# Optimization experiments

Hardware: AMD Instinct MI355X
Metric: run time of the kernel (lower is better)

The kernel has to match this reference:

```python
import jax, jax.numpy as jnp
import numpy as np

A_PER_MOL = 32
N_MOL = 512
N_ATOMS = A_PER_MOL * N_MOL
F = 128
N_RBF = 20
L = 3
CUTOFF = 5.0
ACTION_SCALE = 1.0
ACTION_NORM_LIMIT = 1.0
EPS = 1e-8
MAX_Z = 100


def ssp(x):
    # shifted softplus used throughout schnetpack SchNet
    return jax.nn.softplus(x) - jnp.log(2.0)


def setup_inputs():
    key = jax.random.key(0)
    ks = jax.random.split(key, 12)
    positions = jax.random.normal(ks[0], (N_ATOMS, 3), jnp.float32) * 2.0
    Z = jax.random.randint(ks[1], (N_ATOMS,), 1, MAX_Z)
    # fully-connected intra-molecule neighbor lists (i != j)
    base = np.arange(A_PER_MOL)
    ii, jj = np.meshgrid(base, base, indexing='ij')
    m = ii != jj
    off = (np.arange(N_MOL) * A_PER_MOL)[:, None]
    idx_i = jnp.asarray((ii[m][None, :] + off).reshape(-1))
    idx_j = jnp.asarray((jj[m][None, :] + off).reshape(-1))
    mol_id = jnp.asarray(np.repeat(np.arange(N_MOL), A_PER_MOL))
    emb = jax.random.normal(ks[2], (MAX_Z, F)) * 0.1
    in2f_W = jax.random.normal(ks[3], (L, F, F)) * F ** -0.5
    filt_W1 = jax.random.normal(ks[4], (L, N_RBF, F)) * N_RBF ** -0.5
    filt_b1 = jnp.zeros((L, F))
    filt_W2 = jax.random.normal(ks[5], (L, F, F)) * F ** -0.5
    filt_b2 = jnp.zeros((L, F))
    f2out_W1 = jax.random.normal(ks[6], (L, F, F)) * F ** -0.5
    f2out_b1 = jnp.zeros((L, F))
    f2out_W2 = jax.random.normal(ks[7], (L, F, F)) * F ** -0.5
    f2out_b2 = jnp.zeros((L, F))
    aw_W1 = jax.random.normal(ks[8], (F, F // 2)) * F ** -0.5
    aw_b1 = jnp.zeros((F // 2,))
    aw_W2 = jax.random.normal(ks[9], (F // 2, 1)) * (F // 2) ** -0.5
    aw_b2 = jnp.zeros((1,))
    return dict(positions=positions, emb=emb, in2f_W=in2f_W, filt_W1=filt_W1,
                filt_b1=filt_b1, filt_W2=filt_W2, filt_b2=filt_b2,
                f2out_W1=f2out_W1, f2out_b1=f2out_b1, f2out_W2=f2out_W2,
                f2out_b2=f2out_b2, aw_W1=aw_W1, aw_b1=aw_b1, aw_W2=aw_W2,
                aw_b2=aw_b2, Z=Z, idx_i=idx_i, idx_j=idx_j, mol_id=mol_id)


def _energy(positions, emb, in2f_W, filt_W1, filt_b1, filt_W2, filt_b2,
            f2out_W1, f2out_b1, f2out_W2, f2out_b2, aw_W1, aw_b1, aw_W2,
            aw_b2, Z, idx_i, idx_j, mol_id):
    # PairwiseDistances
    rij = positions[idx_j] - positions[idx_i]                 # [E,3]
    d = jnp.sqrt(jnp.sum(rij * rij, axis=-1) + 1e-12)         # [E]
    # GaussianRBF(0..cutoff, n_rbf)
    offsets = jnp.linspace(0.0, CUTOFF, N_RBF)
    coeff = -0.5 / (offsets[1] - offsets[0]) ** 2
    rbf = jnp.exp(coeff * (d[:, None] - offsets) ** 2)        # [E,n_rbf]
    # CosineCutoff
    fcut = 0.5 * (jnp.cos(jnp.pi * d / CUTOFF) + 1.0) * (d < CUTOFF)
    x = emb[Z]                                                # [N,F]
    for l in range(L):  # SchNet interaction blocks
        h = x @ in2f_W[l]                                     # [N,F]
        Wf = ssp(rbf @ filt_W1[l] + filt_b1[l]) @ filt_W2[l] + filt_b2[l]
        msg = h[idx_j] * (Wf * fcut[:, None])                 # [E,F]
        agg = jax.ops.segment_sum(msg, idx_i, num_segments=N_ATOMS)
        x = x + (ssp(agg @ f2out_W1[l] + f2out_b1[l]) @ f2out_W2[l] + f2out_b2[l])
    # Atomwise energy head + per-molecule sum
    e_atom = (ssp(x @ aw_W1 + aw_b1) @ aw_W2 + aw_b2)[:, 0]   # [N]
    return jax.ops.segment_sum(e_atom, mol_id, num_segments=N_MOL)  # [M]


def reference(positions, emb, in2f_W, filt_W1, filt_b1, filt_W2, filt_b2,
              f2out_W1, f2out_b1, f2out_W2, f2out_b2, aw_W1, aw_b1, aw_W2,
              aw_b2, Z, idx_i, idx_j, mol_id):
    energy, vjp_fn = jax.vjp(
        lambda R: _energy(R, emb, in2f_W, filt_W1, filt_b1, filt_W2, filt_b2,
                          f2out_W1, f2out_b1, f2out_W2, f2out_b2, aw_W1,
                          aw_b1, aw_W2, aw_b2, Z, idx_i, idx_j, mol_id),
        positions)
    (gR,) = vjp_fn(jnp.ones_like(energy))
    action = (-gR) * ACTION_SCALE                             # anti_gradient (Forces module)
    # ragged per-molecule max-norm clip (segment version of the python loop)
    norms = jnp.sqrt(jnp.sum(action * action, axis=-1))       # [N]
    maxn = jax.ops.segment_max(norms, mol_id, num_segments=N_MOL)
    coef = jnp.minimum(ACTION_NORM_LIMIT / jnp.maximum(maxn, EPS), 1.0)
    action = action * coef[mol_id][:, None]
    return action, energy
```

## Files before the change

### kernel.cpp

```cpp
#include <hip/hip_runtime.h>
#include <cstddef>


#define FD     128
#define NRBF   20
#define CUTF   5.0f
#define PI_F   3.14159265358979f
#define PW     136
#define WLSZ   40960
#define W2LSZ  98304
#define APM    32

typedef unsigned short u16;
typedef unsigned int   u32;
typedef __attribute__((ext_vector_type(8))) short bf16x8;
typedef __attribute__((ext_vector_type(4))) float f32x4;

__device__ __forceinline__ float u16f(u16 x){ union{u32 i; float f;} v; v.i=((u32)x)<<16; return v.f; }
__device__ __forceinline__ u16 f16r(float f){ union{float f; u32 i;} v; v.f=f; u32 r=v.i+0x7fffu+((v.i>>16)&1u); return (u16)(r>>16); }
__device__ __forceinline__ float sspf(float x){
  return fmaxf(x,0.f) + __logf(1.f + __expf(-fabsf(x))) - 0.6931471805599453f;
}
__device__ __forceinline__ float sigf(float x){
  return __fdividef(1.f, 1.f + __expf(-x));
}
__device__ __forceinline__ float fcutf(float d){ return (d < CUTF) ? 0.5f*(__cosf(PI_F*d/CUTF)+1.f) : 0.f; }

__global__ __launch_bounds__(256) void k_zero(float* __restrict__ p, int n){
  int i = blockIdx.x*256 + threadIdx.x;
  if(i < n) p[i] = 0.f;
}

__global__ __launch_bounds__(256) void k_embed(const float* __restrict__ emb, const int* __restrict__ Z,
                                               float* __restrict__ X0, int n){
  int idx = blockIdx.x*256 + threadIdx.x;
  if(idx >= n) return;
  int a = idx >> 7, f = idx & 127;
  X0[idx] = emb[Z[a]*FD + f];
}

__global__ __launch_bounds__(256) void k_edge_geom(const float* __restrict__ pos,
    const int* __restrict__ Ii, const int* __restrict__ Ij,
    float* __restrict__ De, float* __restrict__ DBe, int E){
  int e = blockIdx.x*256 + threadIdx.x;
  if(e >= E) return;
  int i = Ii[e], j = Ij[e];
  float dx = pos[j*3+0]-pos[i*3+0];
  float dy = pos[j*3+1]-pos[i*3+1];
  float dz = pos[j*3+2]-pos[i*3+2];
  De[e] = sqrtf(dx*dx+dy*dy+dz*dz + 1e-12f);
  DBe[e] = 0.f;
}

__global__ __launch_bounds__(256) void k_prep(const float* __restrict__ fW1,
    const float* __restrict__ fW2, u16* __restrict__ WB){
  int idx = blockIdx.x*256 + threadIdx.x;
  if(idx >= 3*WLSZ) return;
  int l = idx / WLSZ, r = idx - l*WLSZ;
  const float* W1 = fW1 + l*2560;
  const float* W2 = fW2 + l*16384;
  u16* out = WB + l*WLSZ;
  if(r < 4096){
    int c = r >> 5, k = r & 31;
    out[r] = (k < NRBF) ? f16r(W1[k*128 + c]) : (u16)0;
  } else if(r < 8192){
    int rr = r - 4096;
    int k = rr >> 7, c = rr & 127;
    out[r] = (k < NRBF) ? f16r(W1[k*128 + c]) : (u16)0;
  } else if(r < 24576){
    out[r] = f16r(W2[r - 8192]);
  } else {
    int rr = r - 24576;
    int f = rr >> 7, c = rr & 127;
    out[r] = f16r(W2[c*128 + f]);
  }
}

__global__ __launch_bounds__(256) void k_prep2(const float* __restrict__ in2f,
    const float* __restrict__ oW1, const float* __restrict__ oW2,
    u16* __restrict__ WB2){
  int idx = blockIdx.x*256 + threadIdx.x;
  if(idx >= 3*W2LSZ) return;
  int l = idx / W2LSZ, r = idx - l*W2LSZ;
  int mat = r >> 14, q = r & 16383;
  int n = q >> 7, k = q & 127;
  const float* src = (mat < 2) ? (in2f + l*16384) : (mat < 4) ? (oW1 + l*16384) : (oW2 + l*16384);
  float v = (mat & 1) ? src[n*128 + k] : src[k*128 + n];
  WB2[idx] = f16r(v);
}

__global__ __launch_bounds__(256) void k_gemmb(const float* __restrict__ A,
    const u16* __restrict__ Bn, const float* __restrict__ bias,
    const float* __restrict__ res, const float* __restrict__ mul,
    float* __restrict__ out1, float* __restrict__ out2, int act, int Nr){
  __shared__ u16 sA[32*PW];
  const int tid = threadIdx.x;
  const int rb = blockIdx.x * 32;
  #pragma unroll
  for(int q=0;q<4;q++){
    int e = q*256 + tid;
    int r = e >> 5, c4 = (e & 31)*4;
    int rr = rb + r; if(rr >= Nr) rr = Nr-1;
    float4 v = *(const float4*)(A + (size_t)rr*FD + c4);
    sA[r*PW + c4+0] = f16r(v.x);
    sA[r*PW + c4+1] = f16r(v.y);
    sA[r*PW + c4+2] = f16r(v.z);
    sA[r*PW + c4+3] = f16r(v.w);
  }
  __syncthreads();
  const int w = tid >> 6, lane = tid & 63;
  const int quad = lane >> 4, l16 = lane & 15;
  f32x4 acc[2][2];
  #pragma unroll
  for(int mm=0;mm<2;mm++){ acc[mm][0]=(f32x4){0,0,0,0}; acc[mm][1]=(f32x4){0,0,0,0}; }
  #pragma unroll
  for(int ks=0;ks<4;ks++){
    bf16x8 va[2], vb[2];
    #pragma unroll
    for(int mm=0;mm<2;mm++)
      va[mm] = *(const bf16x8*)&sA[(mm*16+l16)*PW + ks*32 + quad*8];
    #pragma unroll
    for(int p=0;p<2;p++)
      vb[p] = *(const bf16x8*)(Bn + ((2*w+p)*16+l16)*128 + ks*32 + quad*8);
    #pragma unroll
    for(int mm=0;mm<2;mm++)
      #pragma unroll
      for(int p=0;p<2;p++)
        acc[mm][p] = __builtin_amdgcn_mfma_f32_16x16x32_bf16(va[mm], vb[p], acc[mm][p], 0,0,0);
  }
  #pragma unroll
  for(int mm=0;mm<2;mm++)
    #pragma unroll
    for(int p=0;p<2;p++){
      const int f = (2*w+p)*16 + l16;
      float bb = bias ? bias[f] : 0.f;
      #pragma unroll
      for(int r=0;r<4;r++){
        int row = rb + mm*16 + quad*4 + r;
        if(row >= Nr) continue;
        size_t o = (size_t)row*FD + f;
        float y = acc[mm][p][r] + bb;
        if(res) y += res[o];
        if(mul) y *= mul[o];
        if(act){ out1[o] = sspf(y); out2[o] = sigf(y); }
        else out1[o] = y;
      }
    }
}

__global__ __launch_bounds__(256) void k_edge_fwd8(
    const float* __restrict__ h,
    const float* __restrict__ De,
    const u16* __restrict__ W1t, const float* __restrict__ b1,
    const u16* __restrict__ W2t, const float* __restrict__ b2,
    float* __restrict__ agg, int EPM){
  __shared__ u16 srbfb[32*32];
  __shared__ u16 sP [32*PW];
  __shared__ u16 sWf[32*PW];
  __shared__ float sD[32];
  __shared__ float sRed[4*128];
  const int tid = threadIdx.x;
  const int nb = gridDim.x;
  const int P = ((nb & 7) == 0) ? ((blockIdx.x & 7)*(nb >> 3) + (blockIdx.x >> 3)) : blockIdx.x;
  const int m = P >> 5, a = P & 31;
  const int a0 = m*APM;
  const int eb = m*EPM + a*(APM-1);
  if(tid < 32) sD[tid] = (tid < APM-1) ? De[eb + tid] : (CUTF + 1.f);
  __syncthreads();
  const float step = CUTF/19.0f;
  const float coef = -0.5f/(step*step);
  {
    #pragma unroll
    for(int q=0;q<4;q++){
      int idx = q*256 + tid;
      int lt = idx >> 5, k = idx & 31;
      float x = sD[lt] - step*(float)k;
      srbfb[idx] = (k < NRBF) ? f16r(__expf(coef*x*x)) : (u16)0;
    }
  }
  __syncthreads();
  const int w = tid >> 6, lane = tid & 63;
  const int quad = lane >> 4, l16 = lane & 15;
  {
    f32x4 acc[2][2];
    #pragma unroll
    for(int mm=0;mm<2;mm++){ acc[mm][0]=(f32x4){0,0,0,0}; acc[mm][1]=(f32x4){0,0,0,0}; }
    bf16x8 va[2], vb[2];
    #pragma unroll
    for(int mm=0;mm<2;mm++)
      va[mm] = *(const bf16x8*)&srbfb[(mm*16+l16)*32 + quad*8];
    #pragma unroll
    for(int p=0;p<2;p++)
      vb[p] = *(const bf16x8*)(W1t + ((2*w+p)*16+l16)*32 + quad*8);
    #pragma unroll
    for(int mm=0;mm<2;mm++)
      #pragma unroll
      for(int p=0;p<2;p++)
        acc[mm][p] = __builtin_amdgcn_mfma_f32_16x16x32_bf16(va[mm], vb[p], acc[mm][p], 0,0,0);
    #pragma unroll
    for(int mm=0;mm<2;mm++)
      #pragma unroll
      for(int p=0;p<2;p++){
        const int c = (2*w+p)*16 + l16;
        float bb = b1[c];
        #pragma unroll
        for(int r=0;r<4;r++)
          sP[(mm*16+quad*4+r)*PW + c] = f16r(sspf(acc[mm][p][r] + bb));
      }
  }
  __syncthreads();
  {
    f32x4 acc[2][2];
    #pragma unroll
    for(int mm=0;mm<2;mm++){ acc[mm][0]=(f32x4){0,0,0,0}; acc[mm][1]=(f32x4){0,0,0,0}; }
    #pragma unroll
    for(int ks=0;ks<4;ks++){
      bf16x8 va[2], vb[2];
      #pragma unroll
      for(int mm=0;mm<2;mm++)
        va[mm] = *(const bf16x8*)&sP[(mm*16+l16)*PW + ks*32 + quad*8];
      #pragma unroll
      for(int p=0;p<2;p++)
        vb[p] = *(const bf16x8*)(W2t + ((2*w+p)*16+l16)*128 + ks*32 + quad*8);
      #pragma unroll
      for(int mm=0;mm<2;mm++)
        #pragma unroll
        for(int p=0;p<2;p++)
          acc[mm][p] = __builtin_amdgcn_mfma_f32_16x16x32_bf16(va[mm], vb[p], acc[mm][p], 0,0,0);
    }
    #pragma unroll
    for(int mm=0;mm<2;mm++)
      #pragma unroll
      for(int p=0;p<2;p++){
        const int f = (2*w+p)*16 + l16;
        float bb = b2[f];
        #pragma unroll
        for(int r=0;r<4;r++)
          sWf[(mm*16+quad*4+r)*PW + f] = f16r(acc[mm][p][r] + bb);
      }
  }
  __syncthreads();
  {
    float r0 = 0.f, r1 = 0.f;
    #pragma unroll
    for(int s=0;s<8;s++){
      int lt = w*8 + s;
      int j = (lt < APM-1) ? (lt + (lt >= a ? 1 : 0)) : 0;
      float fc = fcutf(sD[lt]);
      const float* hr = h + (size_t)(a0 + j)*FD;
      float w0 = u16f(sWf[lt*PW + lane]);
      float w1 = u16f(sWf[lt*PW + lane + 64]);
      r0 += hr[lane]      * w0 * fc;
      r1 += hr[lane + 64] * w1 * fc;
    }
    sRed[w*128 + lane]      = r0;
    sRed[w*128 + lane + 64] = r1;
  }
  __syncthreads();
  if(tid < 128){
    float v = sRed[tid] + sRed[128+tid] + sRed[256+tid] + sRed[384+tid];
    agg[(size_t)(a0+a)*FD + tid] = v;
  }
}

__global__ __launch_bounds__(256) void k_edge_bwd8(
    const float* __restrict__ h, const float* __restrict__ AB,
    const float* __restrict__ De,
    const u16* __restrict__ W1t, const float* __restrict__ b1,
    const u16* __restrict__ W1b, const u16* __restrict__ W2r,
    const u16* __restrict__ W2t, const float* __restrict__ b2,
    float* __restrict__ DBe, float* __restrict__ HB, int EPM){
  __shared__ u16 srbfb[32*32];
  __shared__ float srbf[32*NRBF];
  __shared__ u16 sP [32*PW];
  __shared__ u16 sWf[32*PW];
  __shared__ float sD[32];
  __shared__ float sRed[4*128];
  __shared__ float sdb[32*2];
  __shared__ float sfb[32];
  const int tid = threadIdx.x;
  const int nb = gridDim.x;
  const int P = ((nb & 7) == 0) ? ((blockIdx.x & 7)*(nb >> 3) + (blockIdx.x >> 3)) : blockIdx.x;
  const int m = P >> 5, a = P & 31;
  const int a0 = m*APM;
  const int eb = m*EPM + a*(APM-1);
  if(tid < 32) sD[tid] = (tid < APM-1) ? De[eb + tid] : (CUTF + 1.f);
  __syncthreads();
  const float step = CUTF/19.0f;
  const float coef = -0.5f/(step*step);
  {
    #pragma unroll
    for(int q=0;q<4;q++){
      int idx = q*256 + tid;
      int lt = idx >> 5, k = idx & 31;
      float x = sD[lt] - step*(float)k;
      if(k < NRBF){
        float v = __expf(coef*x*x);
        srbf[lt*NRBF + k] = v;
        srbfb[idx] = f16r(v);
      } else srbfb[idx] = (u16)0;
    }
  }
  __syncthreads();
  const int w = tid >> 6, lane = tid & 63;
  const int quad = lane >> 4, l16 = lane & 15;
  {
    f32x4 acc[2][2];
    #pragma unroll
    for(int mm=0;mm<2;mm++){ acc[mm][0]=(f32x4){0,0,0,0}; acc[mm][1]=(f32x4){0,0,0,0}; }
    bf16x8 va[2], vb[2];
    #pragma unroll
    for(int mm=0;mm<2;mm++)
      va[mm] = *(const bf16x8*)&srbfb[(mm*16+l16)*32 + quad*8];
    #pragma unroll
    for(int p=0;p<2;p++)
      vb[p] = *(const bf16x8*)(W1t + ((2*w+p)*16+l16)*32 + quad*8);
    #pragma unroll
    for(int mm=0;mm<2;mm++)
      #pragma unroll
      for(int p=0;p<2;p++)
        acc[mm][p] = __builtin_amdgcn_mfma_f32_16x16x32_bf16(va[mm], vb[p], acc[mm][p], 0,0,0);
    #pragma unroll
    for(int mm=0;mm<2;mm++)
      #pragma unroll
      for(int p=0;p<2;p++){
        const int c = (2*w+p)*16 + l16;
        float bb = b1[c];
        #pragma unroll
        for(int r=0;r<4;r++)
          sP[(mm*16+quad*4+r)*PW + c] = f16r(sspf(acc[mm][p][r] + bb));
      }
  }
  __syncthreads();
  {
    f32x4 acc[2][2];
    #pragma unroll
    for(int mm=0;mm<2;mm++){ acc[mm][0]=(f32x4){0,0,0,0}; acc[mm][1]=(f32x4){0,0,0,0}; }
    #pragma unroll
    for(int ks=0;ks<4;ks++){
      bf16x8 va[2], vb[2];
      #pragma unroll
      for(int mm=0;mm<2;mm++)
        va[mm] = *(const bf16x8*)&sP[(mm*16+l16)*PW + ks*32 + quad*8];
      #pragma unroll
      for(int p=0;p<2;p++)
        vb[p] = *(const bf16x8*)(W2t + ((2*w+p)*16+l16)*128 + ks*32 + quad*8);
      #pragma unroll
      for(int mm=0;mm<2;mm++)
        #pragma unroll
        for(int p=0;p<2;p++)
          acc[mm][p] = __builtin_amdgcn_mfma_f32_16x16x32_bf16(va[mm], vb[p], acc[mm][p], 0,0,0);
    }
    #pragma unroll
    for(int mm=0;mm<2;mm++)
      #pragma unroll
      for(int p=0;p<2;p++){
        const int f = (2*w+p)*16 + l16;
        float bb = b2[f];
        #pragma unroll
        for(int r=0;r<4;r++)
          sWf[(mm*16+quad*4+r)*PW + f] = f16r(acc[mm][p][r] + bb);
      }
  }
  __syncthreads();
  {
    float ab0 = AB[(size_t)(a0+a)*FD + lane];
    float ab1 = AB[(size_t)(a0+a)*FD + lane + 64];
    float r0 = 0.f, r1 = 0.f;
    float pfv[8];
    #pragma unroll
    for(int s=0;s<8;s++){
      int lt = w*8 + s;
      int j = (lt < APM-1) ? (lt + (lt >= a ? 1 : 0)) : 0;
      float fc = fcutf(sD[lt]);
      const float* hr  = h  + (size_t)(a0 + j)*FD;
      const float* abr = AB + (size_t)(a0 + j)*FD;
      float h0 = hr[lane], h1 = hr[lane + 64];
      float w0 = u16f(sWf[lt*PW + lane]);
      float w1 = u16f(sWf[lt*PW + lane + 64]);
      r0 += abr[lane]      * w0 * fc;
      r1 += abr[lane + 64] * w1 * fc;
      float g0 = ab0*h0, g1 = ab1*h1;
      sWf[lt*PW + lane]      = f16r(g0*fc);
      sWf[lt*PW + lane + 64] = f16r(g1*fc);
      pfv[s] = g0*w0 + g1*w1;
    }
    #pragma unroll
    for(int d2=1; d2<64; d2<<=1){
      #pragma unroll
      for(int s=0;s<8;s++) pfv[s] += __shfl_xor(pfv[s], d2);
    }
    if(lane == 0){
      #pragma unroll
      for(int s=0;s<8;s++) sfb[w*8 + s] = pfv[s];
    }
    sRed[w*128 + lane]      = r0;
    sRed[w*128 + lane + 64] = r1;
  }
  __syncthreads();
  if(tid < 128){
    float v = sRed[tid] + sRed[128+tid] + sRed[256+tid] + sRed[384+tid];
    HB[(size_t)(a0+a)*FD + tid] = v;
  }
  float tbv[2][2][4];
  {
    f32x4 acc[2][2];
    #pragma unroll
    for(int mm=0;mm<2;mm++){ acc[mm][0]=(f32x4){0,0,0,0}; acc[mm][1]=(f32x4){0,0,0,0}; }
    #pragma unroll
    for(int ks=0;ks<4;ks++){
      bf16x8 va[2], vb[2];
      #pragma unroll
      for(int mm=0;mm<2;mm++)
        va[mm] = *(const bf16x8*)&sWf[(mm*16+l16)*PW + ks*32 + quad*8];
      #pragma unroll
      for(int p=0;p<2;p++)
        vb[p] = *(const bf16x8*)(W2r + ((2*w+p)*16+l16)*128 + ks*32 + quad*8);
      #pragma unroll
      for(int mm=0;mm<2;mm++)
        #pragma unroll
        for(int p=0;p<2;p++)
          acc[mm][p] = __builtin_amdgcn_mfma_f32_16x16x32_bf16(va[mm], vb[p], acc[mm][p], 0,0,0);
    }
    #pragma unroll
    for(int mm=0;mm<2;mm++)
      #pragma unroll
      for(int p=0;p<2;p++){
        const int c = (2*w+p)*16 + l16;
        #pragma unroll
        for(int r=0;r<4;r++){
          float Pv = u16f(sP[(mm*16+quad*4+r)*PW + c]);
          float sig = 1.0f - 0.5f*__expf(-Pv);
          tbv[mm][p][r] = acc[mm][p][r] * sig;
        }
      }
  }
  __syncthreads();
  {
    #pragma unroll
    for(int mm=0;mm<2;mm++)
      #pragma unroll
      for(int p=0;p<2;p++){
        const int c = (2*w+p)*16 + l16;
        #pragma unroll
        for(int r=0;r<4;r++)
          sWf[(mm*16+quad*4+r)*PW + c] = f16r(tbv[mm][p][r]);
      }
  }
  __syncthreads();
  {
    const int m3 = w >> 1, p3 = w & 1;
    f32x4 acc = (f32x4){0,0,0,0};
    #pragma unroll
    for(int ks=0;ks<4;ks++){
      bf16x8 va = *(const bf16x8*)&sWf[(m3*16+l16)*PW + ks*32 + quad*8];
      bf16x8 vb = *(const bf16x8*)(W1b + (p3*16+l16)*128 + ks*32 + quad*8);
      acc = __builtin_amdgcn_mfma_f32_16x16x32_bf16(va, vb, acc, 0,0,0);
    }
    const int kr = p3*16 + l16;
    float s0[4];
    #pragma unroll
    for(int r=0;r<4;r++){
      int lt = m3*16 + quad*4 + r;
      float v = 0.f;
      if(kr < NRBF){
        float x = sD[lt] - step*(float)kr;
        v = acc[r] * srbf[lt*NRBF + kr] * (2.f*coef*x);
      }
      s0[r] = v;
    }
    #pragma unroll
    for(int d2=1; d2<16; d2<<=1){
      #pragma unroll
      for(int r=0;r<4;r++) s0[r] += __shfl_xor(s0[r], d2);
    }
    if(l16 == 0){
      #pragma unroll
      for(int r=0;r<4;r++) sdb[(m3*16+quad*4+r)*2 + p3] = s0[r];
    }
  }
  __syncthreads();
  if(tid < APM-1){
    const float d = sD[tid];
    float dfc = (d < CUTF) ? (-0.5f*(PI_F/CUTF)*__sinf(PI_F*d/CUTF)) : 0.f;
    DBe[eb + tid] += sdb[tid*2+0] + sdb[tid*2+1] + sfb[tid]*dfc;
  }
}

__global__ __launch_bounds__(256) void k_head(const float* __restrict__ X3,
    const float* __restrict__ aW1, const float* __restrict__ ab1,
    const float* __restrict__ aW2, const float* __restrict__ ab2,
    const int* __restrict__ mol, float* __restrict__ Emol, float* __restrict__ XB, int N){
  __shared__ float sx[64*129];
  __shared__ float sg[64*65];
  const int tid = threadIdx.x;
  const int base = blockIdx.x*64;
  for(int q=0;q<8;q++){
    int ee = q*256 + tid;
    int r = ee >> 5, c = (ee & 31)*4;
    int row = base + r; if(row >= N) row = N-1;
    float4 v = *(const float4*)(X3 + (size_t)row*FD + c);
    sx[r*129 + c+0] = v.x; sx[r*129 + c+1] = v.y;
    sx[r*129 + c+2] = v.z; sx[r*129 + c+3] = v.w;
  }
  __syncthreads();
  {
    const int a = tid >> 2, q = tid & 3;
    float u[16];
    #pragma unroll
    for(int cc=0;cc<16;cc++) u[cc] = ab1[q*16 + cc];
    for(int f=0; f<128; f++){
      float xv = sx[a*129 + f];
      const float4* wp = (const float4*)(aW1 + f*64 + q*16);
      float4 w0 = wp[0], w1 = wp[1], w2 = wp[2], w3 = wp[3];
      u[0]+=xv*w0.x; u[1]+=xv*w0.y; u[2]+=xv*w0.z; u[3]+=xv*w0.w;
      u[4]+=xv*w1.x; u[5]+=xv*w1.y; u[6]+=xv*w1.z; u[7]+=xv*w1.w;
      u[8]+=xv*w2.x; u[9]+=xv*w2.y; u[10]+=xv*w2.z; u[11]+=xv*w2.w;
      u[12]+=xv*w3.x; u[13]+=xv*w3.y; u[14]+=xv*w3.z; u[15]+=xv*w3.w;
    }
    float pe = 0.f;
    #pragma unroll
    for(int cc=0;cc<16;cc++){
      int c = q*16 + cc;
      pe += sspf(u[cc])*aW2[c];
      sg[a*65 + c] = sigf(u[cc])*aW2[c];
    }
    pe += __shfl_xor(pe, 1);
    pe += __shfl_xor(pe, 2);
    if(q == 0 && base + a < N) atomicAdd(&Emol[mol[base + a]], pe + ab2[0]);
  }
  __syncthreads();
  {
    const int f = tid & 127, g2 = tid >> 7;
    float acc[32];
    #pragma unroll
    for(int q=0;q<32;q++) acc[q]=0.f;
    for(int c=0;c<64;c++){
      float w = aW1[f*64 + c];
      #pragma unroll
      for(int q=0;q<32;q++) acc[q] += sg[(g2*32+q)*65 + c]*w;
    }
    #pragma unroll
    for(int q=0;q<32;q++){
      int row = base + g2*32 + q;
      if(row < N) XB[(size_t)row*FD + f] = acc[q];
    }
  }
}

__global__ __launch_bounds__(256) void k_grad(const float* __restrict__ pos,
    const int* __restrict__ Ii, const int* __restrict__ Ij,
    const float* __restrict__ De, const float* __restrict__ DBe,
    float* __restrict__ G, int E){
  int e = blockIdx.x*256 + threadIdx.x;
  if(e >= E) return;
  if(De[e] >= CUTF) return;
  float s = DBe[e] / De[e];
  int i = Ii[e], j = Ij[e];
  float dx = s*(pos[i*3+0]-pos[j*3+0]);
  float dy = s*(pos[i*3+1]-pos[j*3+1]);
  float dz = s*(pos[i*3+2]-pos[j*3+2]);
  atomicAdd(&G[i*3+0], dx); atomicAdd(&G[i*3+1], dy); atomicAdd(&G[i*3+2], dz);
  atomicAdd(&G[j*3+0], -dx); atomicAdd(&G[j*3+1], -dy); atomicAdd(&G[j*3+2], -dz);
}

__global__ __launch_bounds__(256) void k_norm(const float* __restrict__ G,
    const int* __restrict__ mol, u32* __restrict__ maxnU, int N){
  int n = blockIdx.x*256 + threadIdx.x;
  if(n >= N) return;
  float ax = G[n*3], ay = G[n*3+1], az = G[n*3+2];
  float nrm = sqrtf(ax*ax+ay*ay+az*az);
  atomicMax(&maxnU[mol[n]], __float_as_uint(nrm));
}

__global__ __launch_bounds__(256) void k_apply(const float* __restrict__ G,
    const int* __restrict__ mol, const u32* __restrict__ maxnU,
    float* __restrict__ outA, int N){
  int n = blockIdx.x*256 + threadIdx.x;
  if(n >= N) return;
  float mx = __uint_as_float(maxnU[mol[n]]);
  float coefc = fminf(1.0f/fmaxf(mx, 1e-8f), 1.0f);
  outA[n*3+0] = -G[n*3+0]*coefc;
  outA[n*3+1] = -G[n*3+1]*coefc;
  outA[n*3+2] = -G[n*3+2]*coefc;
}

extern "C" void kernel_launch(void* const* d_in, const int* in_sizes, int n_in,
                              void* d_out, int out_size, void* d_ws, size_t ws_size,
                              hipStream_t stream) {
  (void)n_in;
  const float* pos  = (const float*)d_in[0];
  const float* emb  = (const float*)d_in[1];
  const float* in2f = (const float*)d_in[2];
  const float* fW1  = (const float*)d_in[3];
  const float* fb1  = (const float*)d_in[4];
  const float* fW2  = (const float*)d_in[5];
  const float* fb2  = (const float*)d_in[6];
  const float* oW1  = (const float*)d_in[7];
  const float* ob1  = (const float*)d_in[8];
  const float* oW2  = (const float*)d_in[9];
  const float* ob2  = (const float*)d_in[10];
  const float* aW1  = (const float*)d_in[11];
  const float* ab1  = (const float*)d_in[12];
  const float* aW2  = (const float*)d_in[13];
  const float* ab2  = (const float*)d_in[14];
  const int*   Z    = (const int*)d_in[15];
  const int*   Ii   = (const int*)d_in[16];
  const int*   Ij   = (const int*)d_in[17];
  const int*   mol  = (const int*)d_in[18];
  const int N = in_sizes[15];
  const int E = in_sizes[16];
  const int M = out_size - N*3;
  const int EPM = E / M;
  const size_t NFE = (size_t)N*FD;
  float* outF = (float*)d_out;
  float* outE = outF + (size_t)N*3;
  float* ws = (float*)d_ws;
  if(ws_size < (11*NFE + 2*(size_t)E + 3*(WLSZ/2) + 3*(W2LSZ/2) + 64)*4) return;

  float* X0  = ws;
  float* SV0 = ws + 4*NFE;
  float* H   = ws + 7*NFE;
  float* AGG = ws + 8*NFE;
  float* XB  = ws + 9*NFE;
  float* HB  = ws + 10*NFE;
  float* De  = ws + 11*NFE;
  float* DBe = De + E;
  u16*   WB  = (u16*)(DBe + E);
  u16*   WB2 = WB + 3*WLSZ;
  float* G    = AGG;
  u32*  maxnU = (u32*)H;

  const int gN   = (int)((NFE + 255)/256);
  const int gE   = (E + 255)/256;
  const int gRow = (N + 31)/32;
  const int gHead= (N + 63)/64;

  k_embed<<<gN,256,0,stream>>>(emb, Z, X0, (int)NFE);
  k_edge_geom<<<gE,256,0,stream>>>(pos, Ii, Ij, De, DBe, E);
  k_prep<<<(3*WLSZ+255)/256,256,0,stream>>>(fW1, fW2, WB);
  k_prep2<<<(3*W2LSZ+255)/256,256,0,stream>>>(in2f, oW1, oW2, WB2);
  for(int l=0;l<3;l++){
    float* Xl  = X0 + (size_t)l*NFE;
    float* Xn  = X0 + (size_t)(l+1)*NFE;
    float* SVl = SV0 + (size_t)l*NFE;
    const u16* W1t = WB + l*WLSZ;
    const u16* W2t = W1t + 24576;
    const u16* d = WB2 + l*W2LSZ;
    const u16 *in2f_t = d, *oW1_t = d + 32768, *oW2_t = d + 65536;
    k_gemmb<<<gRow,256,0,stream>>>(Xl, in2f_t, nullptr, nullptr, nullptr, H, nullptr, 0, N);
    k_edge_fwd8<<<N,256,0,stream>>>(H, De, W1t, fb1 + l*128, W2t, fb2 + l*128, AGG, EPM);
    k_gemmb<<<gRow,256,0,stream>>>(AGG, oW1_t, ob1 + l*128, nullptr, nullptr, H, SVl, 1, N);
    k_gemmb<<<gRow,256,0,stream>>>(H, oW2_t, ob2 + l*128, Xl, nullptr, Xn, nullptr, 0, N);
  }
  k_zero<<<(M+255)/256,256,0,stream>>>(outE, M);
  k_head<<<gHead,256,0,stream>>>(X0 + 3*NFE, aW1, ab1, aW2, ab2, mol, outE, XB, N);
  for(int l=2;l>=0;l--){
    float* Xl  = X0 + (size_t)l*NFE;
    float* SVl = SV0 + (size_t)l*NFE;
    const u16* W1t = WB + l*WLSZ;
    const u16* W1b = W1t + 4096;
    const u16* W2r = W1t + 8192;
    const u16* W2t = W1t + 24576;
    const u16* d = WB2 + l*W2LSZ;
    const u16 *in2f_t = d, *in2f_d = d + 16384, *oW1_d = d + 49152, *oW2_d = d + 81920;
    k_gemmb<<<gRow,256,0,stream>>>(XB, oW2_d, nullptr, nullptr, SVl, AGG, nullptr, 0, N);
    k_gemmb<<<gRow,256,0,stream>>>(AGG, oW1_d, nullptr, nullptr, nullptr, AGG, nullptr, 0, N);
    k_gemmb<<<gRow,256,0,stream>>>(Xl, in2f_t, nullptr, nullptr, nullptr, H, nullptr, 0, N);
    k_edge_bwd8<<<N,256,0,stream>>>(H, AGG, De, W1t, fb1 + l*128, W1b, W2r, W2t, fb2 + l*128, DBe, HB, EPM);
    k_gemmb<<<gRow,256,0,stream>>>(HB, in2f_d, nullptr, XB, nullptr, XB, nullptr, 0, N);
  }
  k_zero<<<(N*3+255)/256,256,0,stream>>>(G, N*3);
  k_zero<<<(M+255)/256,256,0,stream>>>((float*)maxnU, M);
  k_grad<<<gE,256,0,stream>>>(pos, Ii, Ij, De, DBe, G, E);
  k_norm<<<(N+255)/256,256,0,stream>>>(G, mol, maxnU, N);
  k_apply<<<(N+255)/256,256,0,stream>>>(G, mol, maxnU, outF, N);
}
```

Baseline: 1.428 ms.

## Cache forward edge filter activations for reuse in backward edge kernel

The forward edge kernel now stores its per-edge pre-activation (sP) and filter (sWf) tiles in bf16 to a workspace buffer for each layer. A new backward kernel reloads these tiles instead of recomputing the RBF expansion and the two filter-network GEMMs. This trades recomputation for roughly 8 KB of extra global traffic per atom per layer and a large extra workspace allocation. The path is taken only when the workspace is big enough, and otherwise falls back to the old kernel.

```diff
diff --git a/kernel.cpp b/kernel.cpp
--- a/kernel.cpp
+++ b/kernel.cpp
@@ -153,7 +153,7 @@
     const float* __restrict__ De,
     const u16* __restrict__ W1t, const float* __restrict__ b1,
     const u16* __restrict__ W2t, const float* __restrict__ b2,
-    float* __restrict__ agg, int EPM){
+    float* __restrict__ agg, u16* __restrict__ PC, u16* __restrict__ WC, int EPM){
   __shared__ u16 srbfb[32*32];
   __shared__ u16 sP [32*PW];
   __shared__ u16 sWf[32*PW];
@@ -240,6 +240,17 @@
       }
   }
   __syncthreads();
+  if(WC){
+    u16* PCt = PC + (size_t)P*4096;
+    u16* WCt = WC + (size_t)P*4096;
+    #pragma unroll
+    for(int q=0;q<2;q++){
+      int idx = q*256 + tid;
+      int row = idx >> 4, c8 = (idx & 15)*8;
+      *(bf16x8*)(PCt + row*128 + c8) = *(const bf16x8*)&sP[row*PW + c8];
+      *(bf16x8*)(WCt + row*128 + c8) = *(const bf16x8*)&sWf[row*PW + c8];
+    }
+  }
   {
     float r0 = 0.f, r1 = 0.f;
     #pragma unroll
@@ -466,6 +477,166 @@
       if(kr < NRBF){
         float x = sD[lt] - step*(float)kr;
         v = acc[r] * srbf[lt*NRBF + kr] * (2.f*coef*x);
+      }
+      s0[r] = v;
+    }
+    #pragma unroll
+    for(int d2=1; d2<16; d2<<=1){
+      #pragma unroll
+      for(int r=0;r<4;r++) s0[r] += __shfl_xor(s0[r], d2);
+    }
+    if(l16 == 0){
+      #pragma unroll
+      for(int r=0;r<4;r++) sdb[(m3*16+quad*4+r)*2 + p3] = s0[r];
+    }
+  }
+  __syncthreads();
+  if(tid < APM-1){
+    const float d = sD[tid];
+    float dfc = (d < CUTF) ? (-0.5f*(PI_F/CUTF)*__sinf(PI_F*d/CUTF)) : 0.f;
+    DBe[eb + tid] += sdb[tid*2+0] + sdb[tid*2+1] + sfb[tid]*dfc;
+  }
+}
+
+__global__ __launch_bounds__(256) void k_edge_bwd9c(
+    const float* __restrict__ h, const float* __restrict__ AB,
+    const float* __restrict__ De,
+    const u16* __restrict__ PC, const u16* __restrict__ WC,
+    const u16* __restrict__ W1b, const u16* __restrict__ W2r,
+    float* __restrict__ DBe, float* __restrict__ HB, int EPM){
+  __shared__ u16 sP [32*PW];
+  __shared__ u16 sWf[32*PW];
+  __shared__ float sD[32];
+  __shared__ float sRed[4*128];
+  __shared__ float sdb[32*2];
+  __shared__ float sfb[32];
+  const int tid = threadIdx.x;
+  const int nb = gridDim.x;
+  const int P = ((nb & 7) == 0) ? ((blockIdx.x & 7)*(nb >> 3) + (blockIdx.x >> 3)) : blockIdx.x;
+  const int m = P >> 5, a = P & 31;
+  const int a0 = m*APM;
+  const int eb = m*EPM + a*(APM-1);
+  const u16* PCt = PC + (size_t)P*4096;
+  const u16* WCt = WC + (size_t)P*4096;
+  if(tid < 32) sD[tid] = (tid < APM-1) ? De[eb + tid] : (CUTF + 1.f);
+  {
+    #pragma unroll
+    for(int q=0;q<2;q++){
+      int idx = q*256 + tid;
+      int row = idx >> 4, c8 = (idx & 15)*8;
+      *(bf16x8*)&sP [row*PW + c8] = *(const bf16x8*)(PCt + row*128 + c8);
+      *(bf16x8*)&sWf[row*PW + c8] = *(const bf16x8*)(WCt + row*128 + c8);
+    }
+  }
+  __syncthreads();
+  const float step = CUTF/19.0f;
+  const float coef = -0.5f/(step*step);
+  const int w = tid >> 6, lane = tid & 63;
+  const int quad = lane >> 4, l16 = lane & 15;
+  {
+    float ab0 = AB[(size_t)(a0+a)*FD + lane];
+    float ab1 = AB[(size_t)(a0+a)*FD + lane + 64];
+    float r0 = 0.f, r1 = 0.f;
+    float pfv[8];
+    #pragma unroll
+    for(int s=0;s<8;s++){
+      int lt = w*8 + s;
+      int j = (lt < APM-1) ? (lt + (lt >= a ? 1 : 0)) : 0;
+      float fc = fcutf(sD[lt]);
+      const float* hr  = h  + (size_t)(a0 + j)*FD;
+      const float* abr = AB + (size_t)(a0 + j)*FD;
+      float h0 = hr[lane], h1 = hr[lane + 64];
+      float w0 = u16f(sWf[lt*PW + lane]);
+      float w1 = u16f(sWf[lt*PW + lane + 64]);
+      r0 += abr[lane]      * w0 * fc;
+      r1 += abr[lane + 64] * w1 * fc;
+      float g0 = ab0*h0, g1 = ab1*h1;
+      sWf[lt*PW + lane]      = f16r(g0*fc);
+      sWf[lt*PW + lane + 64] = f16r(g1*fc);
+      pfv[s] = g0*w0 + g1*w1;
+    }
+    #pragma unroll
+    for(int d2=1; d2<64; d2<<=1){
+      #pragma unroll
+      for(int s=0;s<8;s++) pfv[s] += __shfl_xor(pfv[s], d2);
+    }
+    if(lane == 0){
+      #pragma unroll
+      for(int s=0;s<8;s++) sfb[w*8 + s] = pfv[s];
+    }
+    sRed[w*128 + lane]      = r0;
+    sRed[w*128 + lane + 64] = r1;
+  }
+  __syncthreads();
+  if(tid < 128){
+    float v = sRed[tid] + sRed[128+tid] + sRed[256+tid] + sRed[384+tid];
+    HB[(size_t)(a0+a)*FD + tid] = v;
+  }
+  float tbv[2][2][4];
+  {
+    f32x4 acc[2][2];
+    #pragma unroll
+    for(int mm=0;mm<2;mm++){ acc[mm][0]=(f32x4){0,0,0,0}; acc[mm][1]=(f32x4){0,0,0,0}; }
+    #pragma unroll
+    for(int ks=0;ks<4;ks++){
+      bf16x8 va[2], vb[2];
+      #pragma unroll
+      for(int mm=0;mm<2;mm++)
+        va[mm] = *(const bf16x8*)&sWf[(mm*16+l16)*PW + ks*32 + quad*8];
+      #pragma unroll
+      for(int p=0;p<2;p++)
+        vb[p] = *(const bf16x8*)(W2r + ((2*w+p)*16+l16)*128 + ks*32 + quad*8);
+      #pragma unroll
+      for(int mm=0;mm<2;mm++)
+        #pragma unroll
+        for(int p=0;p<2;p++)
+          acc[mm][p] = __builtin_amdgcn_mfma_f32_16x16x32_bf16(va[mm], vb[p], acc[mm][p], 0,0,0);
+    }
+    #pragma unroll
+    for(int mm=0;mm<2;mm++)
+      #pragma unroll
+      for(int p=0;p<2;p++){
+        const int c = (2*w+p)*16 + l16;
+        #pragma unroll
+        for(int r=0;r<4;r++){
+          float Pv = u16f(sP[(mm*16+quad*4+r)*PW + c]);
+          float sig = 1.0f - 0.5f*__expf(-Pv);
+          tbv[mm][p][r] = acc[mm][p][r] * sig;
+        }
+      }
+  }
+  __syncthreads();
+  {
+    #pragma unroll
+    for(int mm=0;mm<2;mm++)
+      #pragma unroll
+      for(int p=0;p<2;p++){
+        const int c = (2*w+p)*16 + l16;
+        #pragma unroll
+        for(int r=0;r<4;r++)
+          sWf[(mm*16+quad*4+r)*PW + c] = f16r(tbv[mm][p][r]);
+      }
+  }
+  __syncthreads();
+  {
+    const int m3 = w >> 1, p3 = w & 1;
+    f32x4 acc = (f32x4){0,0,0,0};
+    #pragma unroll
+    for(int ks=0;ks<4;ks++){
+      bf16x8 va = *(const bf16x8*)&sWf[(m3*16+l16)*PW + ks*32 + quad*8];
+      bf16x8 vb = *(const bf16x8*)(W1b + (p3*16+l16)*128 + ks*32 + quad*8);
+      acc = __builtin_amdgcn_mfma_f32_16x16x32_bf16(va, vb, acc, 0,0,0);
+    }
+    const int kr = p3*16 + l16;
+    float s0[4];
+    #pragma unroll
+    for(int r=0;r<4;r++){
+      int lt = m3*16 + quad*4 + r;
+      float v = 0.f;
+      if(kr < NRBF){
+        float x = sD[lt] - step*(float)kr;
+        float rb = __expf(coef*x*x);
+        v = acc[r] * rb * (2.f*coef*x);
       }
       s0[r] = v;
     }
@@ -616,7 +787,10 @@
   float* outF = (float*)d_out;
   float* outE = outF + (size_t)N*3;
   float* ws = (float*)d_ws;
-  if(ws_size < (11*NFE + 2*(size_t)E + 3*(WLSZ/2) + 3*(W2LSZ/2) + 64)*4) return;
+  const size_t base_u32 = 11*NFE + 2*(size_t)E + 3*(WLSZ/2) + 3*(W2LSZ/2) + 64;
+  if(ws_size < base_u32*4) return;
+  const size_t CSZ = (size_t)N*4096;
+  const int fast = (ws_size >= (base_u32 + 3*CSZ + 16)*4);
 
   float* X0  = ws;
   float* SV0 = ws + 4*NFE;
@@ -628,6 +802,8 @@
   float* DBe = De + E;
   u16*   WB  = (u16*)(DBe + E);
   u16*   WB2 = WB + 3*WLSZ;
+  u16*   PC  = WB2 + 3*W2LSZ;
+  u16*   WC  = PC + 3*CSZ;
   float* G    = AGG;
   u32*  maxnU = (u32*)H;
 
@@ -648,8 +824,10 @@
     const u16* W2t = W1t + 24576;
     const u16* d = WB2 + l*W2LSZ;
     const u16 *in2f_t = d, *oW1_t = d + 32768, *oW2_t = d + 65536;
+    u16* PCl = fast ? (PC + l*CSZ) : (u16*)nullptr;
+    u16* WCl = fast ? (WC + l*CSZ) : (u16*)nullptr;
     k_gemmb<<<gRow,256,0,stream>>>(Xl, in2f_t, nullptr, nullptr, nullptr, H, nullptr, 0, N);
-    k_edge_fwd8<<<N,256,0,stream>>>(H, De, W1t, fb1 + l*128, W2t, fb2 + l*128, AGG, EPM);
+    k_edge_fwd8<<<N,256,0,stream>>>(H, De, W1t, fb1 + l*128, W2t, fb2 + l*128, AGG, PCl, WCl, EPM);
     k_gemmb<<<gRow,256,0,stream>>>(AGG, oW1_t, ob1 + l*128, nullptr, nullptr, H, SVl, 1, N);
     k_gemmb<<<gRow,256,0,stream>>>(H, oW2_t, ob2 + l*128, Xl, nullptr, Xn, nullptr, 0, N);
   }
@@ -667,7 +845,11 @@
     k_gemmb<<<gRow,256,0,stream>>>(XB, oW2_d, nullptr, nullptr, SVl, AGG, nullptr, 0, N);
     k_gemmb<<<gRow,256,0,stream>>>(AGG, oW1_d, nullptr, nullptr, nullptr, AGG, nullptr, 0, N);
     k_gemmb<<<gRow,256,0,stream>>>(Xl, in2f_t, nullptr, nullptr, nullptr, H, nullptr, 0, N);
-    k_edge_bwd8<<<N,256,0,stream>>>(H, AGG, De, W1t, fb1 + l*128, W1b, W2r, W2t, fb2 + l*128, DBe, HB, EPM);
+    if(fast){
+      k_edge_bwd9c<<<N,256,0,stream>>>(H, AGG, De, PC + l*CSZ, WC + l*CSZ, W1b, W2r, DBe, HB, EPM);
+    } else {
+      k_edge_bwd8<<<N,256,0,stream>>>(H, AGG, De, W1t, fb1 + l*128, W1b, W2r, W2t, fb2 + l*128, DBe, HB, EPM);
+    }
     k_gemmb<<<gRow,256,0,stream>>>(HB, in2f_d, nullptr, XB, nullptr, XB, nullptr, 0, N);
   }
   k_zero<<<(N*3+255)/256,256,0,stream>>>(G, N*3);
```

After: 1.431 ms. No clear change (+0.2%).
